# Performance work log

Measured on AMD Instinct MI355X. Metric: run time of the kernel, lower is better.

The kernel has to match this reference:

```python
import jax, jax.numpy as jnp
import numpy as np

H = 8        # num_heads
DH = 64      # head_dim
DV = 64      # value_dim
DQ = 256     # query_dim
DHIT = 256   # hit_feature_dim
DMLP = 512   # query_dim * mlp_hidden_dim_multiplier
EPS = 1e-5


def _layernorm(x, g, b):
    m = jnp.mean(x, axis=-1, keepdims=True)
    v = jnp.mean(jnp.square(x - m), axis=-1, keepdims=True)
    return (x - m) * jax.lax.rsqrt(v + EPS) * g + b


def setup_inputs() -> dict:
    key = jax.random.key(0)
    ks = jax.random.split(key, 10)
    B, K, N = 8, 64, 16384
    s = 0.02
    return {
        "slot_representations": jax.random.normal(ks[0], (B, K, DQ), jnp.float32),
        "hit_features": jax.random.normal(ks[1], (B, N, DHIT), jnp.float32),
        "ln1_g": jnp.ones((DQ,), jnp.float32),
        "ln1_b": jnp.zeros((DQ,), jnp.float32),
        "Wq": jax.random.normal(ks[2], (DQ, H * DH), jnp.float32) * s,
        "Wk": jax.random.normal(ks[3], (DHIT, H * DH), jnp.float32) * s,
        "Wv": jax.random.normal(ks[4], (DHIT, H * DV), jnp.float32) * s,
        "W1": jax.random.normal(ks[5], (H * DV, DMLP), jnp.float32) * s,
        "b1": jnp.zeros((DMLP,), jnp.float32),
        "W2": jax.random.normal(ks[6], (DMLP, DQ), jnp.float32) * s,
        "b2": jnp.zeros((DQ,), jnp.float32),
        "ln2_g": jnp.ones((DQ,), jnp.float32),
        "ln2_b": jnp.zeros((DQ,), jnp.float32),
    }


def reference(slot_representations, hit_features, ln1_g, ln1_b, Wq, Wk, Wv,
              W1, b1, W2, b2, ln2_g, ln2_b):
    B, K, _ = slot_representations.shape
    _, N, _ = hit_features.shape
    scale = DH ** -0.5
    slots_norm = _layernorm(slot_representations, ln1_g, ln1_b)
    q = (slots_norm @ Wq).reshape(B, K, H, DH)          # [B,K,H,DH]
    k = (hit_features @ Wk).reshape(B, N, H, DH)        # [B,N,H,DH]
    v = (hit_features @ Wv).reshape(B, N, H, DV)        # [B,N,H,DV]
    logits = jnp.einsum('bkhd,bnhd->bhkn', q, k) * scale
    attn = jax.nn.softmax(logits, axis=-1)              # [B,H,K,N]
    att_v = jnp.einsum('bhkn,bnhd->bkhd', attn, v).reshape(B, K, H * DV)
    mlp_out = jax.nn.relu(att_v @ W1 + b1) @ W2 + b2
    return _layernorm(slot_representations + mlp_out, ln2_g, ln2_b)
```

## Files before the change

kernel.cpp:

```cpp
#include <hip/hip_runtime.h>
#include <hip/hip_bf16.h>

#define HH   8
#define Bb   8
#define Kk   64
#define Nn   16384
#define DQd  256
#define EPSf 1e-5f
#define NCH  32
#define CHK  512
#define SUB  32
#define NSUB (CHK / SUB)

typedef __bf16 bf16_t;
typedef __bf16 bf16x8 __attribute__((ext_vector_type(8)));
typedef __bf16 bf16x4 __attribute__((ext_vector_type(4)));
typedef __bf16 bf16x2 __attribute__((ext_vector_type(2)));
typedef float  f32x4  __attribute__((ext_vector_type(4)));
typedef float  f32x16 __attribute__((ext_vector_type(16)));

#define MFMA16(a, b, c) __builtin_amdgcn_mfma_f32_16x16x32_bf16((a), (b), (c), 0, 0, 0)
#define MFMA32(a, b, c) __builtin_amdgcn_mfma_f32_32x32x16_bf16((a), (b), (c), 0, 0, 0)

static __device__ __forceinline__ int pk2(float x, float y) {
    bf16x2 v; v[0] = (bf16_t)x; v[1] = (bf16_t)y;
    return __builtin_bit_cast(int, v);
}

static __device__ __forceinline__ void pack_tile(const f32x16 Sv, int hi, bf16x8* out) {
    #pragma unroll
    for (int kc = 0; kc < 2; ++kc) {
        const int oc = kc * 8;
        int Lp0 = pk2(Sv[oc + 0], Sv[oc + 1]);
        int Lp1 = pk2(Sv[oc + 2], Sv[oc + 3]);
        int Hp0 = pk2(Sv[oc + 4], Sv[oc + 5]);
        int Hp1 = pk2(Sv[oc + 6], Sv[oc + 7]);
        int Lx0 = __shfl_xor(Lp0, 32, 64);
        int Lx1 = __shfl_xor(Lp1, 32, 64);
        int Hx0 = __shfl_xor(Hp0, 32, 64);
        int Hx1 = __shfl_xor(Hp1, 32, 64);
        int4 bi;
        bi.x = hi ? Hx0 : Lp0;
        bi.y = hi ? Hx1 : Lp1;
        bi.z = hi ? Hp0 : Lx0;
        bi.w = hi ? Hp1 : Lx1;
        out[kc] = __builtin_bit_cast(bf16x8, bi);
    }
}

static __device__ __forceinline__ void store8(bf16_t* dst, float4 a, float4 b) {
    bf16x8 o;
    o[0] = (bf16_t)a.x; o[1] = (bf16_t)a.y; o[2] = (bf16_t)a.z; o[3] = (bf16_t)a.w;
    o[4] = (bf16_t)b.x; o[5] = (bf16_t)b.y; o[6] = (bf16_t)b.z; o[7] = (bf16_t)b.w;
    *(bf16x8*)dst = o;
}

__global__ __launch_bounds__(256) void k1_qt(
    const float* __restrict__ slots, const float* __restrict__ g1,
    const float* __restrict__ bb1, const float* __restrict__ Wq,
    const float* __restrict__ Wk, const float* __restrict__ Wv,
    bf16_t* __restrict__ qt, bf16_t* __restrict__ WvT)
{
    __shared__ alignas(16) bf16_t nrow[64][264];
    __shared__ alignas(16) bf16_t wqT[64][264];
    __shared__ alignas(16) bf16_t qb[64][72];
    __shared__ alignas(16) bf16_t wkT[256][72];

    if (blockIdx.x >= 64) {
        const int h = blockIdx.x - 64;
        const int t = threadIdx.x;
        const int dv = t & 63, dq = t >> 6;
        #pragma unroll
        for (int i = 0; i < 16; ++i) {
            int d = dq * 64 + i * 4;
            bf16x4 o;
            #pragma unroll
            for (int j = 0; j < 4; ++j)
                o[j] = (bf16_t)Wv[(size_t)(d + j) * 512 + h * 64 + dv];
            *(bf16x4*)&WvT[(size_t)(h * 64 + dv) * 256 + d] = o;
        }
        return;
    }

    const int b = blockIdx.x >> 3, h = blockIdx.x & 7;
    const int t = threadIdx.x;
    const int w = t >> 6, lane = t & 63;
    const int l15 = lane & 15, quad = lane >> 4;

    {
        float4 gv = *(const float4*)&g1[lane * 4];
        float4 bv = *(const float4*)&bb1[lane * 4];
        for (int i = 0; i < 16; ++i) {
            int row = w * 16 + i;
            float4 x = *(const float4*)&slots[((size_t)b * Kk + row) * DQd + lane * 4];
            float s = x.x + x.y + x.z + x.w;
            for (int m = 1; m < 64; m <<= 1) s += __shfl_xor(s, m, 64);
            float mean = s * (1.0f / 256.0f);
            float dx = x.x - mean, dy = x.y - mean, dz = x.z - mean, dw = x.w - mean;
            float v2 = dx * dx + dy * dy + dz * dz + dw * dw;
            for (int m = 1; m < 64; m <<= 1) v2 += __shfl_xor(v2, m, 64);
            float rs = rsqrtf(v2 * (1.0f / 256.0f) + EPSf);
            bf16x4 o;
            o[0] = (bf16_t)(dx * rs * gv.x + bv.x);
            o[1] = (bf16_t)(dy * rs * gv.y + bv.y);
            o[2] = (bf16_t)(dz * rs * gv.z + bv.z);
            o[3] = (bf16_t)(dw * rs * gv.w + bv.w);
            *(bf16x4*)&nrow[row][lane * 4] = o;
        }
    }
    {
        int d = t & 63, r4 = t >> 6;
        #pragma unroll 8
        for (int p = 0; p < 64; ++p) {
            int i = r4 + p * 4;
            wqT[d][i] = (bf16_t)Wq[(size_t)i * 512 + h * 64 + d];
            wkT[i][d] = (bf16_t)Wk[(size_t)i * 512 + h * 64 + d];
        }
    }
    __syncthreads();

    f32x4 acc1[4] = {};
    for (int ks = 0; ks < 8; ++ks) {
        bf16x8 a = *(const bf16x8*)&nrow[w * 16 + l15][ks * 32 + quad * 8];
        #pragma unroll
        for (int tt = 0; tt < 4; ++tt) {
            bf16x8 bfr = *(const bf16x8*)&wqT[tt * 16 + l15][ks * 32 + quad * 8];
            acc1[tt] = MFMA16(a, bfr, acc1[tt]);
        }
    }
    #pragma unroll
    for (int tt = 0; tt < 4; ++tt)
        #pragma unroll
        for (int r = 0; r < 4; ++r)
            qb[w * 16 + quad * 4 + r][tt * 16 + l15] = (bf16_t)(acc1[tt][r] * 0.125f);
    __syncthreads();

    f32x4 acc2[16] = {};
    for (int ks = 0; ks < 2; ++ks) {
        bf16x8 a = *(const bf16x8*)&qb[w * 16 + l15][ks * 32 + quad * 8];
        #pragma unroll
        for (int tt = 0; tt < 16; ++tt) {
            bf16x8 bfr = *(const bf16x8*)&wkT[tt * 16 + l15][ks * 32 + quad * 8];
            acc2[tt] = MFMA16(a, bfr, acc2[tt]);
        }
    }
    size_t base = (size_t)(b * HH + h) * 64;
    #pragma unroll
    for (int tt = 0; tt < 16; ++tt)
        #pragma unroll
        for (int r = 0; r < 4; ++r)
            qt[(base + w * 16 + quad * 4 + r) * 256 + tt * 16 + l15] = (bf16_t)acc2[tt][r];
}

__global__ __launch_bounds__(512) void k3_attn(
    const float* __restrict__ hit, const bf16_t* __restrict__ qt,
    const bf16_t* __restrict__ WvT, bf16_t* __restrict__ nump,
    float* __restrict__ lp)
{
    __shared__ alignas(16) bf16_t hs[2][SUB * 256];
    __shared__ alignas(16) bf16_t vb[2][16 * 512];

    const int bid = blockIdx.x;
    const int c  = bid & 31;
    const int hg = (bid >> 5) & 1;
    const int b  = bid >> 6;
    const int t  = threadIdx.x;
    const int w = t >> 6, lane = t & 63;
    const int l31 = lane & 31, hi = lane >> 5;
    const int hl = w >> 1;
    const int qh = w & 1;
    const int h  = hg * 4 + hl;
    const int bh = b * HH + h;

    bf16x8 qf[16], wf[16];
    {
        const bf16_t* qrow = qt + ((size_t)bh * 64 + qh * 32 + l31) * 256 + hi * 8;
        const bf16_t* wrow = WvT + ((size_t)(h * 64 + qh * 32 + l31)) * 256 + hi * 8;
        #pragma unroll
        for (int ks = 0; ks < 16; ++ks) {
            qf[ks] = *(const bf16x8*)(qrow + ks * 16);
            wf[ks] = *(const bf16x8*)(wrow + ks * 16);
        }
    }

    f32x16 accO = {};
    f32x16 accX = {};
    float ls = 0.f;

    const float* hbase = hit + ((size_t)b * Nn + c * CHK) * 256;
    const int row0 = t >> 5, g0 = t & 31;
    const int sw0 = (g0 ^ (row0 & 7)) * 8;
    const int sw1 = (g0 ^ ((row0 + 16) & 7)) * 8;

    float4 pA0, pA1, pB0, pB1;
#define PREFETCH(ss) do { \
        const float* s0_ = hbase + (size_t)(ss) * SUB * 256 + (size_t)row0 * 256 + g0 * 8; \
        pA0 = ((const float4*)s0_)[0]; pA1 = ((const float4*)s0_)[1]; \
        const float* s1_ = s0_ + 16 * 256; \
        pB0 = ((const float4*)s1_)[0]; pB1 = ((const float4*)s1_)[1]; \
    } while (0)

    PREFETCH(0);
    store8(&hs[0][row0 * 256 + sw0], pA0, pA1);
    store8(&hs[0][(row0 + 16) * 256 + sw1], pB0, pB1);
    PREFETCH(1);
    __syncthreads();

    const int xr = l31 & 7;

    for (int s = 0; s < NSUB; ++s) {
        const int cur = s & 1;
        const bf16_t* hrow = &hs[cur][l31 * 256];

        f32x16 St = {}, Vt = {};
        #pragma unroll
        for (int ks = 0; ks < 16; ++ks) {
            bf16x8 A = *(const bf16x8*)(hrow + (((2 * ks + hi) ^ xr) * 8));
            Vt = MFMA32(A, wf[ks], Vt);
            St = MFMA32(A, qf[ks], St);
        }

        if (s + 1 < NSUB) {
            store8(&hs[cur ^ 1][row0 * 256 + sw0], pA0, pA1);
            store8(&hs[cur ^ 1][(row0 + 16) * 256 + sw1], pB0, pB1);
        }
        if (s + 2 < NSUB) PREFETCH(s + 2);

        #pragma unroll
        for (int r = 0; r < 16; ++r) {
            float e = __expf(St[r]);
            St[r] = e;
            ls += e;
        }
        bf16x8 Pf[2];
        pack_tile(St, hi, Pf);
        {
            bf16x8 Vf[2];
            pack_tile(Vt, hi, Vf);
            *(bf16x8*)&vb[cur][((hl * 2 + 0) * 2 + qh) * 512 + lane * 8] = Vf[0];
            *(bf16x8*)&vb[cur][((hl * 2 + 1) * 2 + qh) * 512 + lane * 8] = Vf[1];
        }
        __syncthreads();

        {
            bf16x8 vo0 = *(const bf16x8*)&vb[cur][((hl * 2 + 0) * 2 + qh) * 512 + lane * 8];
            bf16x8 vx0 = *(const bf16x8*)&vb[cur][((hl * 2 + 0) * 2 + (1 - qh)) * 512 + lane * 8];
            bf16x8 vo1 = *(const bf16x8*)&vb[cur][((hl * 2 + 1) * 2 + qh) * 512 + lane * 8];
            bf16x8 vx1 = *(const bf16x8*)&vb[cur][((hl * 2 + 1) * 2 + (1 - qh)) * 512 + lane * 8];
            accO = MFMA32(Pf[0], vo0, accO);
            accX = MFMA32(Pf[0], vx0, accX);
            accO = MFMA32(Pf[1], vo1, accO);
            accX = MFMA32(Pf[1], vx1, accX);
        }
    }
#undef PREFETCH

    {
        float lt = ls + __shfl_xor(ls, 32, 64);
        if (hi == 0)
            lp[((size_t)bh * NCH + c) * 64 + qh * 32 + l31] = lt;
    }
    {
        size_t nbase = ((size_t)bh * NCH + c) * 64 * 64;
        #pragma unroll
        for (int r = 0; r < 16; ++r) {
            int q = qh * 32 + (r & 3) + 8 * (r >> 2) + 4 * hi;
            size_t ro = nbase + (size_t)q * 64;
            nump[ro + qh * 32 + l31]       = (bf16_t)accO[r];
            nump[ro + (1 - qh) * 32 + l31] = (bf16_t)accX[r];
        }
    }
}

__global__ __launch_bounds__(512) void k35_comb(
    const bf16_t* __restrict__ nump, const float* __restrict__ lp,
    bf16_t* __restrict__ X)
{
    const int bh = blockIdx.x, b = bh >> 3, h = bh & 7;
    const int t = threadIdx.x;
    const int q = t >> 3, g = t & 7;
    float s8[8] = {};
    float lsum = 0.f;
    #pragma unroll 4
    for (int cc = 0; cc < NCH; ++cc) {
        size_t base = ((size_t)bh * NCH + cc) * 64 + q;
        bf16x8 v = *(const bf16x8*)&nump[base * 64 + g * 8];
        #pragma unroll
        for (int j = 0; j < 8; ++j) s8[j] += (float)v[j];
        lsum += lp[base];
    }
    float inv = 1.0f / lsum;
    bf16x8 o;
    #pragma unroll
    for (int j = 0; j < 8; ++j) o[j] = (bf16_t)(s8[j] * inv);
    *(bf16x8*)&X[((size_t)b * 64 + q) * 512 + h * 64 + g * 8] = o;
}

__global__ __launch_bounds__(256) void k4a_mlp1(
    const bf16_t* __restrict__ X, const float* __restrict__ W1,
    const float* __restrict__ b1, bf16_t* __restrict__ H)
{
    __shared__ alignas(16) bf16_t Xs[64 * 512];
    __shared__ float scr4[4][32 * 33];

    const int rt = blockIdx.x >> 3, ct = blockIdx.x & 7;
    const int t = threadIdx.x;
    {
        const int row = t >> 2, c0 = t & 3;
        const bf16_t* src = X + ((size_t)rt * 64 + row) * 512;
        #pragma unroll
        for (int i = 0; i < 16; ++i) {
            int cc = c0 + i * 4;
            bf16x8 v = *(const bf16x8*)(src + cc * 8);
            *(bf16x8*)&Xs[row * 512 + ((cc ^ (row & 7)) * 8)] = v;
        }
    }
    __syncthreads();

    const int w = t >> 6, lane = t & 63, l31 = lane & 31, hi = lane >> 5;
    const int mr = w >> 1, mc = w & 1;
    const int colbase = ct * 64 + mc * 32;
    f32x16 acc = {};
    for (int kc = 0; kc < 32; ++kc) {
        bf16x8 af;
        #pragma unroll
        for (int j = 0; j < 8; ++j)
            af[j] = (bf16_t)W1[(size_t)(kc * 16 + hi * 8 + j) * 512 + colbase + l31];
        int row = mr * 32 + l31;
        int cc = kc * 2 + hi;
        bf16x8 bfr = *(const bf16x8*)&Xs[row * 512 + ((cc ^ (row & 7)) * 8)];
        acc = MFMA32(af, bfr, acc);
    }
    float* scr = scr4[w];
    const float bia = b1[colbase + l31];
    #pragma unroll
    for (int r = 0; r < 16; ++r) {
        int m = (r & 3) + 8 * (r >> 2) + 4 * hi;
        scr[m * 33 + l31] = acc[r];
    }
    #pragma unroll
    for (int j = 0; j < 16; ++j) {
        float v = scr[l31 * 33 + hi * 16 + j] + bia;
        v = fmaxf(v, 0.f);
        H[((size_t)rt * 64 + mr * 32 + hi * 16 + j) * 512 + colbase + l31] = (bf16_t)v;
    }
}

__global__ __launch_bounds__(256) void k4b_gemm(
    const bf16_t* __restrict__ H, const float* __restrict__ W2,
    const float* __restrict__ b2, const float* __restrict__ slots,
    float* __restrict__ ys)
{
    __shared__ alignas(16) bf16_t Hs[64 * 512];
    __shared__ float scr4[4][32 * 33];

    const int b = blockIdx.x >> 2, ct = blockIdx.x & 3;
    const int t = threadIdx.x;
    {
        const int row = t >> 2, c0 = t & 3;
        const bf16_t* src = H + ((size_t)b * 64 + row) * 512;
        #pragma unroll
        for (int i = 0; i < 16; ++i) {
            int cc = c0 + i * 4;
            bf16x8 v = *(const bf16x8*)(src + cc * 8);
            *(bf16x8*)&Hs[row * 512 + ((cc ^ (row & 7)) * 8)] = v;
        }
    }
    __syncthreads();

    const int w = t >> 6, lane = t & 63, l31 = lane & 31, hi = lane >> 5;
    const int mr = w >> 1, mc = w & 1;
    const int colbase = ct * 64 + mc * 32;
    f32x16 acc = {};
    for (int kc = 0; kc < 32; ++kc) {
        bf16x8 af;
        #pragma unroll
        for (int j = 0; j < 8; ++j)
            af[j] = (bf16_t)W2[(size_t)(kc * 16 + hi * 8 + j) * 256 + colbase + l31];
        int row = mr * 32 + l31;
        int cc = kc * 2 + hi;
        bf16x8 bfr = *(const bf16x8*)&Hs[row * 512 + ((cc ^ (row & 7)) * 8)];
        acc = MFMA32(af, bfr, acc);
    }
    float* scr = scr4[w];
    const float b2c = b2[colbase + l31];
    #pragma unroll
    for (int r = 0; r < 16; ++r) {
        int m = (r & 3) + 8 * (r >> 2) + 4 * hi;
        scr[m * 33 + l31] = acc[r];
    }
    #pragma unroll
    for (int j = 0; j < 16; ++j) {
        int rowl = mr * 32 + hi * 16 + j;
        float v = scr[l31 * 33 + hi * 16 + j] + b2c
                + slots[((size_t)b * 64 + rowl) * 256 + colbase + l31];
        ys[((size_t)b * 64 + rowl) * 256 + colbase + l31] = v;
    }
}

__global__ __launch_bounds__(256) void k4c_ln2(
    const float* __restrict__ ys, const float* __restrict__ g2,
    const float* __restrict__ bb2, float* __restrict__ out)
{
    const int t = threadIdx.x;
    const int w = t >> 6, lane = t & 63;
    float4 gv = *(const float4*)&g2[lane * 4];
    float4 bv = *(const float4*)&bb2[lane * 4];
    #pragma unroll
    for (int rr = 0; rr < 2; ++rr) {
        int row = blockIdx.x * 8 + w * 2 + rr;
        float4 x = *(const float4*)&ys[(size_t)row * 256 + lane * 4];
        float s = x.x + x.y + x.z + x.w;
        for (int m = 1; m < 64; m <<= 1) s += __shfl_xor(s, m, 64);
        float mean = s * (1.0f / 256.0f);
        float dx = x.x - mean, dy = x.y - mean, dz = x.z - mean, dw = x.w - mean;
        float v2 = dx * dx + dy * dy + dz * dz + dw * dw;
        for (int m = 1; m < 64; m <<= 1) v2 += __shfl_xor(v2, m, 64);
        float rs = rsqrtf(v2 * (1.0f / 256.0f) + EPSf);
        float4 o;
        o.x = dx * rs * gv.x + bv.x;
        o.y = dy * rs * gv.y + bv.y;
        o.z = dz * rs * gv.z + bv.z;
        o.w = dw * rs * gv.w + bv.w;
        *(float4*)&out[(size_t)row * 256 + lane * 4] = o;
    }
}

extern "C" void kernel_launch(void* const* d_in, const int* in_sizes, int n_in,
                              void* d_out, int out_size, void* d_ws, size_t ws_size,
                              hipStream_t stream) {
    (void)in_sizes; (void)n_in; (void)out_size; (void)ws_size;
    const float* slots = (const float*)d_in[0];
    const float* hit   = (const float*)d_in[1];
    const float* g1    = (const float*)d_in[2];
    const float* bb1   = (const float*)d_in[3];
    const float* Wq    = (const float*)d_in[4];
    const float* Wk    = (const float*)d_in[5];
    const float* Wv    = (const float*)d_in[6];
    const float* W1    = (const float*)d_in[7];
    const float* b1v   = (const float*)d_in[8];
    const float* W2    = (const float*)d_in[9];
    const float* b2v   = (const float*)d_in[10];
    const float* g2    = (const float*)d_in[11];
    const float* bb2   = (const float*)d_in[12];
    float* out = (float*)d_out;

    char* wsp = (char*)d_ws;
    bf16_t* qt   = (bf16_t*)wsp;
    float*  ys   = (float*) wsp;
    bf16_t* WvT  = (bf16_t*)(wsp + (size_t)2097152);
    bf16_t* nump = (bf16_t*)(wsp + (size_t)2359296);
    float*  lp   = (float*) (wsp + (size_t)19136512);
    bf16_t* X    = (bf16_t*)(wsp + (size_t)19660800);
    bf16_t* H    = (bf16_t*)(wsp + (size_t)20185088);

    hipLaunchKernelGGL(k1_qt, dim3(72), dim3(256), 0, stream,
                       slots, g1, bb1, Wq, Wk, Wv, qt, WvT);
    hipLaunchKernelGGL(k3_attn, dim3(Bb * 2 * NCH), dim3(512), 0, stream,
                       hit, qt, WvT, nump, lp);
    hipLaunchKernelGGL(k35_comb, dim3(64), dim3(512), 0, stream,
                       nump, lp, X);
    hipLaunchKernelGGL(k4a_mlp1, dim3(64), dim3(256), 0, stream,
                       X, W1, b1v, H);
    hipLaunchKernelGGL(k4b_gemm, dim3(32), dim3(256), 0, stream,
                       H, W2, b2v, slots, ys);
    hipLaunchKernelGGL(k4c_ln2, dim3(64), dim3(256), 0, stream,
                       ys, g2, bb2, out);
}
```

Before: 304.5 us.

## Fold log2e into Q scale, reorder attention MFMAs, split MLP kernels into smaller blocks

Folds log2(e) into the query scale so the softmax can use exp2f instead of __expf, splits the row-sum accumulator into two, and moves the shared-memory store and prefetch ahead of the MFMA loop with s_setprio around the MFMA sections. The combine and both MLP GEMM kernels are relaunched with more, smaller single-wave blocks that read operands directly from global memory rather than staging them in LDS. The aim is to cut exp cost, improve overlap in the attention loop, and spread the tail kernels over more CUs. The price is extra global-memory traffic in the MLP kernels.

```diff
diff --git a/kernel.cpp b/kernel.cpp
--- a/kernel.cpp
+++ b/kernel.cpp
@@ -21,6 +21,8 @@
 
 #define MFMA16(a, b, c) __builtin_amdgcn_mfma_f32_16x16x32_bf16((a), (b), (c), 0, 0, 0)
 #define MFMA32(a, b, c) __builtin_amdgcn_mfma_f32_32x32x16_bf16((a), (b), (c), 0, 0, 0)
+
+#define QSCALE 0.1803368801111f
 
 static __device__ __forceinline__ int pk2(float x, float y) {
     bf16x2 v; v[0] = (bf16_t)x; v[1] = (bf16_t)y;
@@ -90,6 +92,7 @@
     {
         float4 gv = *(const float4*)&g1[lane * 4];
         float4 bv = *(const float4*)&bb1[lane * 4];
+        #pragma unroll 2
         for (int i = 0; i < 16; ++i) {
             int row = w * 16 + i;
             float4 x = *(const float4*)&slots[((size_t)b * Kk + row) * DQd + lane * 4];
@@ -132,7 +135,7 @@
     for (int tt = 0; tt < 4; ++tt)
         #pragma unroll
         for (int r = 0; r < 4; ++r)
-            qb[w * 16 + quad * 4 + r][tt * 16 + l15] = (bf16_t)(acc1[tt][r] * 0.125f);
+            qb[w * 16 + quad * 4 + r][tt * 16 + l15] = (bf16_t)(acc1[tt][r] * QSCALE);
     __syncthreads();
 
     f32x4 acc2[16] = {};
@@ -185,7 +188,7 @@
 
     f32x16 accO = {};
     f32x16 accX = {};
-    float ls = 0.f;
+    float ls0 = 0.f, ls1 = 0.f;
 
     const float* hbase = hit + ((size_t)b * Nn + c * CHK) * 256;
     const int row0 = t >> 5, g0 = t & 31;
@@ -212,25 +215,27 @@
         const int cur = s & 1;
         const bf16_t* hrow = &hs[cur][l31 * 256];
 
-        f32x16 St = {}, Vt = {};
-        #pragma unroll
-        for (int ks = 0; ks < 16; ++ks) {
-            bf16x8 A = *(const bf16x8*)(hrow + (((2 * ks + hi) ^ xr) * 8));
-            Vt = MFMA32(A, wf[ks], Vt);
-            St = MFMA32(A, qf[ks], St);
-        }
-
         if (s + 1 < NSUB) {
             store8(&hs[cur ^ 1][row0 * 256 + sw0], pA0, pA1);
             store8(&hs[cur ^ 1][(row0 + 16) * 256 + sw1], pB0, pB1);
         }
         if (s + 2 < NSUB) PREFETCH(s + 2);
 
+        f32x16 St = {}, Vt = {};
+        __builtin_amdgcn_s_setprio(1);
+        #pragma unroll
+        for (int ks = 0; ks < 16; ++ks) {
+            bf16x8 A = *(const bf16x8*)(hrow + (((2 * ks + hi) ^ xr) * 8));
+            St = MFMA32(A, qf[ks], St);
+            Vt = MFMA32(A, wf[ks], Vt);
+        }
+        __builtin_amdgcn_s_setprio(0);
+
         #pragma unroll
         for (int r = 0; r < 16; ++r) {
-            float e = __expf(St[r]);
+            float e = exp2f(St[r]);
             St[r] = e;
-            ls += e;
+            if (r & 1) ls1 += e; else ls0 += e;
         }
         bf16x8 Pf[2];
         pack_tile(St, hi, Pf);
@@ -242,6 +247,7 @@
         }
         __syncthreads();
 
+        __builtin_amdgcn_s_setprio(1);
         {
             bf16x8 vo0 = *(const bf16x8*)&vb[cur][((hl * 2 + 0) * 2 + qh) * 512 + lane * 8];
             bf16x8 vx0 = *(const bf16x8*)&vb[cur][((hl * 2 + 0) * 2 + (1 - qh)) * 512 + lane * 8];
@@ -252,10 +258,12 @@
             accO = MFMA32(Pf[1], vo1, accO);
             accX = MFMA32(Pf[1], vx1, accX);
         }
+        __builtin_amdgcn_s_setprio(0);
     }
 #undef PREFETCH
 
     {
+        float ls = ls0 + ls1;
         float lt = ls + __shfl_xor(ls, 32, 64);
         if (hi == 0)
             lp[((size_t)bh * NCH + c) * 64 + qh * 32 + l31] = lt;
@@ -272,13 +280,14 @@
     }
 }
 
-__global__ __launch_bounds__(512) void k35_comb(
+__global__ __launch_bounds__(256) void k35_comb(
     const bf16_t* __restrict__ nump, const float* __restrict__ lp,
     bf16_t* __restrict__ X)
 {
-    const int bh = blockIdx.x, b = bh >> 3, h = bh & 7;
+    const int bh = blockIdx.x >> 1, qhb = blockIdx.x & 1;
+    const int b = bh >> 3, h = bh & 7;
     const int t = threadIdx.x;
-    const int q = t >> 3, g = t & 7;
+    const int q = qhb * 32 + (t >> 3), g = t & 7;
     float s8[8] = {};
     float lsum = 0.f;
     #pragma unroll 4
@@ -296,105 +305,76 @@
     *(bf16x8*)&X[((size_t)b * 64 + q) * 512 + h * 64 + g * 8] = o;
 }
 
-__global__ __launch_bounds__(256) void k4a_mlp1(
+__global__ __launch_bounds__(64) void k4a_mlp1(
     const bf16_t* __restrict__ X, const float* __restrict__ W1,
     const float* __restrict__ b1, bf16_t* __restrict__ H)
 {
-    __shared__ alignas(16) bf16_t Xs[64 * 512];
-    __shared__ float scr4[4][32 * 33];
-
-    const int rt = blockIdx.x >> 3, ct = blockIdx.x & 7;
-    const int t = threadIdx.x;
-    {
-        const int row = t >> 2, c0 = t & 3;
-        const bf16_t* src = X + ((size_t)rt * 64 + row) * 512;
-        #pragma unroll
-        for (int i = 0; i < 16; ++i) {
-            int cc = c0 + i * 4;
-            bf16x8 v = *(const bf16x8*)(src + cc * 8);
-            *(bf16x8*)&Xs[row * 512 + ((cc ^ (row & 7)) * 8)] = v;
-        }
-    }
-    __syncthreads();
-
-    const int w = t >> 6, lane = t & 63, l31 = lane & 31, hi = lane >> 5;
-    const int mr = w >> 1, mc = w & 1;
-    const int colbase = ct * 64 + mc * 32;
+    __shared__ float scr[32 * 33];
+    const int rt = blockIdx.x >> 4, ct = blockIdx.x & 15;
+    const int lane = threadIdx.x, l31 = lane & 31, hi = lane >> 5;
+    const int colbase = ct * 32;
+
+    const bf16_t* xrow = X + ((size_t)(rt * 32 + l31)) * 512 + hi * 8;
     f32x16 acc = {};
+    #pragma unroll 4
     for (int kc = 0; kc < 32; ++kc) {
         bf16x8 af;
         #pragma unroll
         for (int j = 0; j < 8; ++j)
             af[j] = (bf16_t)W1[(size_t)(kc * 16 + hi * 8 + j) * 512 + colbase + l31];
-        int row = mr * 32 + l31;
-        int cc = kc * 2 + hi;
-        bf16x8 bfr = *(const bf16x8*)&Xs[row * 512 + ((cc ^ (row & 7)) * 8)];
+        bf16x8 bfr = *(const bf16x8*)(xrow + kc * 16);
         acc = MFMA32(af, bfr, acc);
     }
-    float* scr = scr4[w];
     const float bia = b1[colbase + l31];
     #pragma unroll
     for (int r = 0; r < 16; ++r) {
         int m = (r & 3) + 8 * (r >> 2) + 4 * hi;
         scr[m * 33 + l31] = acc[r];
     }
+    __syncthreads();
     #pragma unroll
     for (int j = 0; j < 16; ++j) {
         float v = scr[l31 * 33 + hi * 16 + j] + bia;
         v = fmaxf(v, 0.f);
-        H[((size_t)rt * 64 + mr * 32 + hi * 16 + j) * 512 + colbase + l31] = (bf16_t)v;
-    }
-}
-
-__global__ __launch_bounds__(256) void k4b_gemm(
+        H[((size_t)(rt * 32 + hi * 16 + j)) * 512 + colbase + l31] = (bf16_t)v;
+    }
+}
+
+__global__ __launch_bounds__(64) void k4b_gemm(
     const bf16_t* __restrict__ H, const float* __restrict__ W2,
     const float* __restrict__ b2, const float* __restrict__ slots,
     float* __restrict__ ys)
 {
-    __shared__ alignas(16) bf16_t Hs[64 * 512];
-    __shared__ float scr4[4][32 * 33];
-
-    const int b = blockIdx.x >> 2, ct = blockIdx.x & 3;
-    const int t = threadIdx.x;
-    {
-        const int row = t >> 2, c0 = t & 3;
-        const bf16_t* src = H + ((size_t)b * 64 + row) * 512;
-        #pragma unroll
-        for (int i = 0; i < 16; ++i) {
-            int cc = c0 + i * 4;
-            bf16x8 v = *(const bf16x8*)(src + cc * 8);
-            *(bf16x8*)&Hs[row * 512 + ((cc ^ (row & 7)) * 8)] = v;
-        }
-    }
-    __syncthreads();
-
-    const int w = t >> 6, lane = t & 63, l31 = lane & 31, hi = lane >> 5;
-    const int mr = w >> 1, mc = w & 1;
-    const int colbase = ct * 64 + mc * 32;
+    __shared__ float scr[32 * 33];
+    const int b = blockIdx.x >> 4, rtt = (blockIdx.x >> 3) & 1, ct = blockIdx.x & 7;
+    const int lane = threadIdx.x, l31 = lane & 31, hi = lane >> 5;
+    const int colbase = ct * 32;
+    const int rowbase = b * 64 + rtt * 32;
+
+    const bf16_t* hrow = H + ((size_t)(rowbase + l31)) * 512 + hi * 8;
     f32x16 acc = {};
+    #pragma unroll 4
     for (int kc = 0; kc < 32; ++kc) {
         bf16x8 af;
         #pragma unroll
         for (int j = 0; j < 8; ++j)
             af[j] = (bf16_t)W2[(size_t)(kc * 16 + hi * 8 + j) * 256 + colbase + l31];
-        int row = mr * 32 + l31;
-        int cc = kc * 2 + hi;
-        bf16x8 bfr = *(const bf16x8*)&Hs[row * 512 + ((cc ^ (row & 7)) * 8)];
+        bf16x8 bfr = *(const bf16x8*)(hrow + kc * 16);
         acc = MFMA32(af, bfr, acc);
     }
-    float* scr = scr4[w];
     const float b2c = b2[colbase + l31];
     #pragma unroll
     for (int r = 0; r < 16; ++r) {
         int m = (r & 3) + 8 * (r >> 2) + 4 * hi;
         scr[m * 33 + l31] = acc[r];
     }
+    __syncthreads();
     #pragma unroll
     for (int j = 0; j < 16; ++j) {
-        int rowl = mr * 32 + hi * 16 + j;
+        int row = rowbase + hi * 16 + j;
         float v = scr[l31 * 33 + hi * 16 + j] + b2c
-                + slots[((size_t)b * 64 + rowl) * 256 + colbase + l31];
-        ys[((size_t)b * 64 + rowl) * 256 + colbase + l31] = v;
+                + slots[(size_t)row * 256 + colbase + l31];
+        ys[(size_t)row * 256 + colbase + l31] = v;
     }
 }
 
@@ -458,11 +438,11 @@
                        slots, g1, bb1, Wq, Wk, Wv, qt, WvT);
     hipLaunchKernelGGL(k3_attn, dim3(Bb * 2 * NCH), dim3(512), 0, stream,
                        hit, qt, WvT, nump, lp);
-    hipLaunchKernelGGL(k35_comb, dim3(64), dim3(512), 0, stream,
+    hipLaunchKernelGGL(k35_comb, dim3(128), dim3(256), 0, stream,
                        nump, lp, X);
-    hipLaunchKernelGGL(k4a_mlp1, dim3(64), dim3(256), 0, stream,
+    hipLaunchKernelGGL(k4a_mlp1, dim3(256), dim3(64), 0, stream,
                        X, W1, b1v, H);
-    hipLaunchKernelGGL(k4b_gemm, dim3(32), dim3(256), 0, stream,
+    hipLaunchKernelGGL(k4b_gemm, dim3(128), dim3(64), 0, stream,
                        H, W2, b2v, slots, ys);
     hipLaunchKernelGGL(k4c_ln2, dim3(64), dim3(256), 0, stream,
                        ys, g2, bb2, out);
```

After: 413.0 us. 1.36x slower.
